# Performance work log

Hardware: AMD Instinct MI355X
Metric: run time of the kernel (lower is better)

## Reference

```python
import jax, jax.numpy as jnp
import numpy as np
import math

S = 72; IMG_W = 640; IMG_H = 360; STRIDE = 16
IN_CH = 256; AFC = 64
FMAP_H = IMG_H // STRIDE  # 22
FMAP_W = IMG_W // STRIDE  # 40
N_OFFSETS = S
LEFT_ANGLES = [72., 60., 49., 39., 30., 22.]
RIGHT_ANGLES = [108., 120., 131., 141., 150., 158.]
BOTTOM_ANGLES = [165., 150., 141., 131., 120., 108., 100., 90., 80., 72., 60., 49., 39., 30., 15.]
BATCH = 8


def _gen_anchor(start, angle, cut):
    n = FMAP_H if cut else N_OFFSETS
    ys = np.linspace(1., 0., n)
    a = np.zeros(5 + n)
    sx, sy = start
    a[2] = 1. - sy
    a[3] = sx
    a[5:] = (sx + (1. - ys - 1. + sy) / math.tan(angle * math.pi / 180.)) * IMG_W
    return a


def _gen_side(angles, nb, x=None, y=None):
    if x is None:
        starts = [(xx, y) for xx in np.linspace(1., 0., nb)]
    else:
        starts = [(x, yy) for yy in np.linspace(1., 0., nb)]
    anc = np.stack([_gen_anchor(s, a, False) for s in starts for a in angles])
    cut = np.stack([_gen_anchor(s, a, True) for s in starts for a in angles])
    return anc, cut


def build_anchor_tables():
    la, lc = _gen_side(LEFT_ANGLES, 72, x=0.)
    ra, rc = _gen_side(RIGHT_ANGLES, 72, x=1.)
    ba, bc = _gen_side(BOTTOM_ANGLES, 128, y=1.)
    anchors = np.concatenate([la, ba, ra]).astype(np.float32)  # [P, 5+S]
    cuts = np.concatenate([lc, bc, rc])                        # [P, 5+fmap_h]
    xs = np.flip(np.round(cuts[:, 5:] / STRIDE), axis=1).astype(np.int64)
    cut_xs = np.clip(xs, 0, FMAP_W - 1).astype(np.int32)       # [P, fmap_h]
    invalid = (xs < 0) | (xs > FMAP_W)                         # faithful to original (> not >=)
    return anchors, cut_xs, invalid


def setup_inputs():
    key = jax.random.key(0)
    ks = jax.random.split(key, 6)
    anchors, cut_xs, invalid = build_anchor_tables()
    P = anchors.shape[0]  # 2784
    D = AFC * FMAP_H      # 1408
    s = 0.02
    return {
        "x": jax.random.normal(ks[0], (BATCH, IN_CH, FMAP_H, FMAP_W), jnp.float32),
        "conv_w": jax.random.normal(ks[1], (AFC, IN_CH), jnp.float32) * s,
        "conv_b": jnp.zeros((AFC,), jnp.float32),
        "att_w": jax.random.normal(ks[2], (P - 1, D), jnp.float32) * s,
        "att_b": jnp.zeros((P - 1,), jnp.float32),
        "cls_w": jax.random.normal(ks[3], (2, 2 * D), jnp.float32) * s,
        "cls_b": jnp.zeros((2,), jnp.float32),
        "so_w": jax.random.normal(ks[4], (1, 2 * D), jnp.float32) * s,
        "so_b": jnp.zeros((1,), jnp.float32),
        "reg_w": jax.random.normal(ks[5], (N_OFFSETS + 1, 2 * D), jnp.float32) * s,
        "reg_b": jnp.zeros((N_OFFSETS + 1,), jnp.float32),
        "anchors": jnp.asarray(anchors),
        "cut_xs": jnp.asarray(cut_xs),
        "invalid_mask": jnp.asarray(invalid),
    }


def reference(x, conv_w, conv_b, att_w, att_b, cls_w, cls_b, so_w, so_b, reg_w, reg_b, anchors, cut_xs, invalid_mask):
    B = x.shape[0]
    P, H = cut_xs.shape
    # 1x1 conv
    feat = jnp.einsum('bchw,oc->bohw', x, conv_w) + conv_b[None, :, None, None]
    # fused anchor feature gather: rois[b,p,c,h] = feat[b,c,h,cut_xs[p,h]]
    rois = feat[:, :, jnp.arange(H)[None, :], cut_xs]           # [B,C,P,H]
    rois = jnp.transpose(rois, (0, 2, 1, 3))                    # [B,P,C,H]
    rois = jnp.where(invalid_mask[None, :, None, :], 0., rois)
    D = rois.shape[2] * H
    baf = rois.reshape(B, P, D)
    scores = baf.reshape(B * P, D) @ att_w.T + att_b
    attention = jax.nn.softmax(scores, axis=1).reshape(B, P, P - 1)
    # off-diagonal scatter (replaces torch eye/nonzero trick): M[b,i,j]=attention[b,i,j'] for j!=i, diag 0
    i_idx = jnp.arange(P)[:, None]
    j_off = jnp.arange(P - 1)[None, :]
    tgt_j = jnp.where(j_off < i_idx, j_off, j_off + 1)          # [P,P-1]
    M = jnp.zeros((B, P, P), x.dtype).at[:, jnp.broadcast_to(i_idx, (P, P - 1)), tgt_j].set(attention)
    # (baf^T @ M^T)^T == M @ baf
    att_feats = jnp.einsum('bpq,bqd->bpd', M, baf)
    feats = jnp.concatenate([att_feats, baf], axis=2).reshape(B * P, 2 * D)
    cls = (feats @ cls_w.T + cls_b).reshape(B, P, 2)
    so = jax.nn.sigmoid(feats @ so_w.T + so_b).reshape(B, P, 1)
    reg = (feats @ reg_w.T + reg_b).reshape(B, P, N_OFFSETS + 1)
    anc = jnp.broadcast_to(anchors[None], (B, P, anchors.shape[1]))
    reg_proposals = jnp.concatenate([cls, (anc[:, :, 2:3] + so) * 0.5, anc[:, :, 3:4], anc[:, :, 4:] + reg], axis=2)
    return reg_proposals, M, feat
```

## Files before the change

kernel.cpp:

```cpp
#include <hip/hip_runtime.h>
#include <stdint.h>

#define PTOT 2784
#define PM1  2783
#define DDIM 1408
#define NB   8
#define ROWS 22272
#define KHEAD 2816
#define MROW 2816
#define BTROWS 1536

typedef __attribute__((ext_vector_type(8))) short bf16x8;
typedef __attribute__((ext_vector_type(4))) float f32x4;
typedef long i64f8;

__device__ __forceinline__ short f2bf_rne(float x) {
    uint32_t u = __float_as_uint(x);
    u += 0x7fffu + ((u >> 16) & 1u);
    return (short)(u >> 16);
}
__device__ __forceinline__ float bf2f(short s) {
    return __uint_as_float((uint32_t)(unsigned short)s << 16);
}

__device__ __forceinline__ unsigned char f2e4m3(float x) {
    uint32_t u = __float_as_uint(x);
    uint32_t sgn = (u >> 24) & 0x80u;
    uint32_t ax = u & 0x7fffffffu;
    ax += 0x7ffffu + ((ax >> 20) & 1u);
    if (ax >= 0x43E80000u) return (unsigned char)(sgn | 0x7Eu);
    if (ax < 0x3C800000u) return (unsigned char)sgn;
    uint32_t e = (ax >> 23) - 120u;
    uint32_t m = (ax >> 20) & 7u;
    return (unsigned char)(sgn | (e << 3) | m);
}

__device__ __forceinline__ void gld16(const void* g, void* l) {
    __builtin_amdgcn_global_load_lds(
        (const __attribute__((address_space(1))) void*)(uintptr_t)g,
        (__attribute__((address_space(3))) void*)(uint32_t)(uintptr_t)l,
        16, 0, 0);
}

__global__ __launch_bounds__(256) void k_conv(
    const float* __restrict__ x, const float* __restrict__ w,
    const float* __restrict__ cb, float* __restrict__ feat) {
  __shared__ float xs[256 * 32];
  int b = blockIdx.x / 28;
  int t0 = (blockIdx.x % 28) * 32;
  int t = threadIdx.x;
  for (int i = t; i < 256 * 32; i += 256) {
    int c = i >> 5, pos = i & 31;
    int hw = t0 + pos;
    xs[i] = (hw < 880) ? x[((size_t)b * 256 + c) * 880 + hw] : 0.f;
  }
  __syncthreads();
  int o = t & 63, g = t >> 6;
  float acc[8];
#pragma unroll
  for (int pp = 0; pp < 8; ++pp) acc[pp] = cb[o];
  const float* wr = w + o * 256;
  for (int c = 0; c < 256; ++c) {
    float wv = wr[c];
#pragma unroll
    for (int pp = 0; pp < 8; ++pp) acc[pp] += wv * xs[c * 32 + g + pp * 4];
  }
#pragma unroll
  for (int pp = 0; pp < 8; ++pp) {
    int hw = t0 + g + pp * 4;
    if (hw < 880) feat[((size_t)b * 64 + o) * 880 + hw] = acc[pp];
  }
}

__global__ __launch_bounds__(256) void k_prep(
    const float* __restrict__ att_w, const float* __restrict__ cls_w,
    const float* __restrict__ so_w, const float* __restrict__ reg_w,
    const float* __restrict__ cls_b, const float* __restrict__ so_b,
    const float* __restrict__ reg_b,
    short* __restrict__ attw, short* __restrict__ wbf,
    float* __restrict__ bias80, float* __restrict__ M,
    unsigned char* __restrict__ Mbf8, unsigned char* __restrict__ bafT8,
    short* __restrict__ Msc) {
  const int64_t n_attw = (int64_t)2816 * DDIM;
  const int64_t n_w = 80 * (int64_t)KHEAD;
  const int64_t n_pa = (int64_t)NB * MROW * 32;
  const int64_t n_pb = (int64_t)NB * BTROWS * 32;
  const int64_t total = n_attw + n_w + 80 + ROWS + n_pa + n_pb;
  for (int64_t i = (int64_t)blockIdx.x * 256 + threadIdx.x; i < total;
       i += (int64_t)gridDim.x * 256) {
    if (i < n_attw) {
      int j = (int)(i / DDIM), k = (int)(i - (int64_t)j * DDIM);
      float v = (j < PM1) ? att_w[(size_t)j * DDIM + k] : 0.f;
      attw[i] = f2bf_rne(v);
    } else if (i < n_attw + n_w) {
      int64_t ii = i - n_attw;
      int n = (int)(ii / KHEAD), k = (int)(ii - (int64_t)n * KHEAD);
      float v = 0.f;
      if (n < 2) v = cls_w[n * KHEAD + k];
      else if (n == 2) v = so_w[k];
      else if (n < 76) v = reg_w[(size_t)(n - 3) * KHEAD + k];
      wbf[ii] = f2bf_rne(v);
    } else if (i < n_attw + n_w + 80) {
      int n = (int)(i - n_attw - n_w);
      float v = 0.f;
      if (n < 2) v = cls_b[n];
      else if (n == 2) v = so_b[0];
      else if (n < 76) v = reg_b[n - 3];
      bias80[n] = v;
    } else if (i < n_attw + n_w + 80 + ROWS) {
      int r = (int)(i - n_attw - n_w - 80);
      int p = r % PTOT;
      M[(size_t)r * PTOT + p] = -1e30f;
      if (Msc) Msc[(size_t)r * PTOT + p] = f2bf_rne(-1e30f);
    } else if (i < n_attw + n_w + 80 + ROWS + n_pa) {
      int64_t ii = i - n_attw - n_w - 80 - ROWS;
      int64_t row = ii >> 5; int c = (int)(ii & 31);
      Mbf8[row * 2816 + 2784 + c] = 0;
    } else {
      int64_t ii = i - n_attw - n_w - 80 - ROWS - n_pa;
      int64_t row = ii >> 5; int c = (int)(ii & 31);
      bafT8[row * 2816 + 2784 + c] = 0;
    }
  }
}

__global__ __launch_bounds__(256) void k_gather(
    const float* __restrict__ feat, const int* __restrict__ cutx,
    const unsigned char* __restrict__ inval,
    short* __restrict__ baf, unsigned char* __restrict__ bafT8) {
  int p0 = blockIdx.x * 64, d0 = blockIdx.y * 64, b = blockIdx.z;
  __shared__ short tile[64][72];
  int t = threadIdx.x;
  for (int i = t; i < 64 * 64; i += 256) {
    int pl = i >> 6, dl = i & 63;
    int p = p0 + pl, d = d0 + dl;
    float v = 0.f;
    if (p < PTOT && d < DDIM) {
      int c = d / 22, h = d - c * 22;
      if (!inval[p * 22 + h]) {
        int xc = cutx[p * 22 + h];
        v = feat[(((size_t)b * 64 + c) * 22 + h) * 40 + xc];
      }
    }
    tile[pl][dl] = f2bf_rne(v);
  }
  __syncthreads();
  if (d0 < DDIM) {
    for (int u = t; u < 512; u += 256) {
      int pl = u >> 3, dg = u & 7;
      int p = p0 + pl;
      if (p < PTOT) {
        bf16x8 v;
#pragma unroll
        for (int e = 0; e < 8; ++e) v[e] = tile[pl][dg * 8 + e];
        *(bf16x8*)&baf[((size_t)b * PTOT + p) * DDIM + d0 + dg * 8] = v;
      }
    }
  }
  for (int u = t; u < 512; u += 256) {
    int dl = u >> 3, pg = u & 7;
    int pbase = p0 + pg * 8;
    if (pbase + 7 < PTOT) {
      unsigned long long pk = 0;
#pragma unroll
      for (int e = 0; e < 8; ++e) {
        float fv = bf2f(tile[pg * 8 + e][dl]);
        pk |= (unsigned long long)f2e4m3(fv) << (8 * e);
      }
      *(unsigned long long*)&bafT8[((size_t)b * BTROWS + d0 + dl) * 2816 + pbase] = pk;
    }
  }
}

template<int OUTMODE>
__global__ __launch_bounds__(256) void k_scores(
    const short* __restrict__ baf, const short* __restrict__ attw,
    const float* __restrict__ att_b, float* __restrict__ Mout,
    short* __restrict__ Msc) {
  __shared__ char smA[8192];
  __shared__ char smB[8192];
  int wg = blockIdx.x;
  int xcd = wg & 7, lin = wg >> 3;
  int wgid = (xcd < 4) ? xcd * 479 + lin : 1916 + (xcd - 4) * 478 + lin;
  int it = wgid / 22, nt = wgid - it * 22;
  int m0 = it * 128, n0 = nt * 128;

  int t = threadIdx.x, w = t >> 6, l = t & 63;
  int lr = l & 15, lg = l >> 4;
  int wr = w >> 1, wc = w & 1;

  const char* gA[2]; const char* gB[2]; int dd[2];
#pragma unroll
  for (int c = 0; c < 2; ++c) {
    int o = w * 2048 + c * 1024 + l * 16;
    int row = o >> 6;
    int colb = (o & 63) ^ (((o >> 7) & 3) << 4);
    gA[c] = (const char*)(baf + (size_t)(m0 + row) * DDIM) + colb;
    gB[c] = (const char*)(attw + (size_t)(n0 + row) * DDIM) + colb;
    dd[c] = o;
  }
  int offA[4], offB[4];
#pragma unroll
  for (int i = 0; i < 4; ++i) {
    int xa = (wr * 64 + i * 16 + lr) * 64 + lg * 16;
    offA[i] = xa ^ (((xa >> 7) & 3) << 4);
    int xb = (wc * 64 + i * 16 + lr) * 64 + lg * 16;
    offB[i] = xb ^ (((xb >> 7) & 3) << 4);
  }

  f32x4 acc[4][4];
  const f32x4 fz = {0.f, 0.f, 0.f, 0.f};
#pragma unroll
  for (int mi = 0; mi < 4; ++mi)
#pragma unroll
    for (int ni = 0; ni < 4; ++ni) acc[mi][ni] = fz;

  for (int kt = 0; kt < 44; ++kt) {
    gld16(gA[0] + (size_t)kt * 64, smA + dd[0]);
    gld16(gA[1] + (size_t)kt * 64, smA + dd[1]);
    gld16(gB[0] + (size_t)kt * 64, smB + dd[0]);
    gld16(gB[1] + (size_t)kt * 64, smB + dd[1]);
    __syncthreads();
    bf16x8 av[4], bv[4];
#pragma unroll
    for (int i = 0; i < 4; ++i) av[i] = *(const bf16x8*)(smA + offA[i]);
#pragma unroll
    for (int i = 0; i < 4; ++i) bv[i] = *(const bf16x8*)(smB + offB[i]);
#pragma unroll
    for (int mi = 0; mi < 4; ++mi)
#pragma unroll
      for (int ni = 0; ni < 4; ++ni)
        acc[mi][ni] = __builtin_amdgcn_mfma_f32_16x16x32_bf16(
            av[mi], bv[ni], acc[mi][ni], 0, 0, 0);
    __syncthreads();
  }

#pragma unroll
  for (int mi = 0; mi < 4; ++mi) {
#pragma unroll
    for (int rg = 0; rg < 4; ++rg) {
      int gmi = m0 + wr * 64 + mi * 16 + lg * 4 + rg;
      int i = gmi % PTOT;
#pragma unroll
      for (int ni = 0; ni < 4; ++ni) {
        int j = n0 + wc * 64 + ni * 16 + lr;
        if (j < PM1) {
          int q2 = j + (j >= i);
          float v = acc[mi][ni][rg] + att_b[j];
          if (OUTMODE == 0) Mout[(size_t)gmi * PTOT + q2] = v;
          else              Msc[(size_t)gmi * PTOT + q2] = f2bf_rne(v);
        }
      }
    }
  }
}

__global__ __launch_bounds__(256) void k_attfeat8(
    const unsigned char* __restrict__ Mbf8,
    const unsigned char* __restrict__ bafT8,
    short* __restrict__ attf) {
  __shared__ char smA[8192];
  __shared__ char smB[8192];
  int wg = blockIdx.x;
  int wgid = (wg & 7) * 242 + (wg >> 3);
  int bb = wgid / 242;
  int rem = wgid - bb * 242;
  int it = rem / 11, nt = rem - it * 11;
  int m0 = it * 128, n0 = nt * 128;
  const unsigned char* Ab = Mbf8 + ((size_t)bb * MROW + m0) * 2816;
  const unsigned char* Bb = bafT8 + ((size_t)bb * BTROWS + n0) * 2816;

  int t = threadIdx.x, w = t >> 6, l = t & 63;
  int lr = l & 15, lg = l >> 4;
  int wr = w >> 1, wc = w & 1;

  const char* gA[2]; const char* gB[2]; int dd[2];
#pragma unroll
  for (int c = 0; c < 2; ++c) {
    int o = c * 4096 + t * 16;
    int row = o >> 6;
    int colb = (o & 63) ^ (((o >> 7) & 3) << 4);
    gA[c] = (const char*)Ab + (size_t)row * 2816 + colb;
    gB[c] = (const char*)Bb + (size_t)row * 2816 + colb;
    dd[c] = o;
  }
  int offA[8], offB[8];
#pragma unroll
  for (int i = 0; i < 4; ++i) {
#pragma unroll
    for (int ks = 0; ks < 2; ++ks) {
      int xa = (wr * 64 + i * 16 + lr) * 64 + ks * 32 + lg * 8;
      offA[i * 2 + ks] = xa ^ (((xa >> 7) & 3) << 4);
      int xb = (wc * 64 + i * 16 + lr) * 64 + ks * 32 + lg * 8;
      offB[i * 2 + ks] = xb ^ (((xb >> 7) & 3) << 4);
    }
  }

  f32x4 acc[4][4];
  const f32x4 fz = {0.f, 0.f, 0.f, 0.f};
#pragma unroll
  for (int mi = 0; mi < 4; ++mi)
#pragma unroll
    for (int ni = 0; ni < 4; ++ni) acc[mi][ni] = fz;

  for (int kt = 0; kt < 44; ++kt) {
    gld16(gA[0] + (size_t)kt * 64, smA + dd[0]);
    gld16(gA[1] + (size_t)kt * 64, smA + dd[1]);
    gld16(gB[0] + (size_t)kt * 64, smB + dd[0]);
    gld16(gB[1] + (size_t)kt * 64, smB + dd[1]);
    __syncthreads();
#pragma unroll
    for (int ks = 0; ks < 2; ++ks) {
      i64f8 av[4], bv[4];
#pragma unroll
      for (int i = 0; i < 4; ++i) av[i] = *(const i64f8*)(smA + offA[i * 2 + ks]);
#pragma unroll
      for (int i = 0; i < 4; ++i) bv[i] = *(const i64f8*)(smB + offB[i * 2 + ks]);
#pragma unroll
      for (int mi = 0; mi < 4; ++mi)
#pragma unroll
        for (int ni = 0; ni < 4; ++ni)
          acc[mi][ni] = __builtin_amdgcn_mfma_f32_16x16x32_fp8_fp8(
              av[mi], bv[ni], acc[mi][ni], 0, 0, 0);
    }
    __syncthreads();
  }

  const float US = 1.0f / 1024.0f;
#pragma unroll
  for (int mi = 0; mi < 4; ++mi) {
#pragma unroll
    for (int rg = 0; rg < 4; ++rg) {
      int i = m0 + wr * 64 + mi * 16 + lg * 4 + rg;
      if (i < PTOT) {
        short* arow = attf + ((size_t)(bb * PTOT + i)) * DDIM + n0 + wc * 64;
#pragma unroll
        for (int ni = 0; ni < 4; ++ni)
          arow[ni * 16 + lr] = f2bf_rne(acc[mi][ni][rg] * US);
      }
    }
  }
}

template<int INMODE>
__global__ __launch_bounds__(256) void k_softmax(float* __restrict__ M,
                                                 unsigned char* __restrict__ Mbf8,
                                                 const short* __restrict__ Msc) {
  __shared__ float red[8];
  int r = blockIdx.x;
  int b = r / PTOT, p = r - b * PTOT;
  float* pr = M + (size_t)r * PTOT;
  const short* ms = INMODE ? (Msc + (size_t)r * PTOT) : (const short*)nullptr;
  unsigned char* mb = Mbf8 + ((size_t)b * MROW + p) * 2816;
  int t = threadIdx.x;
  bool has2 = (t < 348 - 256);
  float v0[8], v1[8];
  float mx = -3.0e38f;
  if (INMODE == 0) {
    f32x4 a0 = *(const f32x4*)(pr + t * 8);
    f32x4 a1 = *(const f32x4*)(pr + t * 8 + 4);
#pragma unroll
    for (int e = 0; e < 4; ++e) { v0[e] = a0[e]; v0[4 + e] = a1[e]; }
  } else {
    bf16x8 a = *(const bf16x8*)(ms + t * 8);
#pragma unroll
    for (int e = 0; e < 8; ++e) v0[e] = bf2f(a[e]);
  }
#pragma unroll
  for (int e = 0; e < 8; ++e) mx = fmaxf(mx, v0[e]);
  if (has2) {
    if (INMODE == 0) {
      f32x4 b0 = *(const f32x4*)(pr + (256 + t) * 8);
      f32x4 b1 = *(const f32x4*)(pr + (256 + t) * 8 + 4);
#pragma unroll
      for (int e = 0; e < 4; ++e) { v1[e] = b0[e]; v1[4 + e] = b1[e]; }
    } else {
      bf16x8 bb = *(const bf16x8*)(ms + (256 + t) * 8);
#pragma unroll
      for (int e = 0; e < 8; ++e) v1[e] = bf2f(bb[e]);
    }
#pragma unroll
    for (int e = 0; e < 8; ++e) mx = fmaxf(mx, v1[e]);
  }
#pragma unroll
  for (int off = 32; off; off >>= 1) mx = fmaxf(mx, __shfl_xor(mx, off));
  if ((t & 63) == 0) red[t >> 6] = mx;
  __syncthreads();
  mx = fmaxf(fmaxf(red[0], red[1]), fmaxf(red[2], red[3]));
  float s = 0.f;
#pragma unroll
  for (int e = 0; e < 8; ++e) { v0[e] = __expf(v0[e] - mx); s += v0[e]; }
  if (has2) {
#pragma unroll
    for (int e = 0; e < 8; ++e) { v1[e] = __expf(v1[e] - mx); s += v1[e]; }
  }
#pragma unroll
  for (int off = 32; off; off >>= 1) s += __shfl_xor(s, off);
  if ((t & 63) == 0) red[4 + (t >> 6)] = s;
  __syncthreads();
  s = (red[4] + red[5]) + (red[6] + red[7]);
  float inv = 1.f / s;
  float invs = inv * 1024.f;
  {
    f32x4 o0, o1; unsigned long long pk = 0;
#pragma unroll
    for (int e = 0; e < 8; ++e) {
      float wv = v0[e] * inv;
      if (e < 4) o0[e] = wv; else o1[e - 4] = wv;
      pk |= (unsigned long long)f2e4m3(v0[e] * invs) << (8 * e);
    }
    *(f32x4*)(pr + t * 8) = o0;
    *(f32x4*)(pr + t * 8 + 4) = o1;
    *(unsigned long long*)(mb + t * 8) = pk;
  }
  if (has2) {
    f32x4 o0, o1; unsigned long long pk = 0;
#pragma unroll
    for (int e = 0; e < 8; ++e) {
      float wv = v1[e] * inv;
      if (e < 4) o0[e] = wv; else o1[e - 4] = wv;
      pk |= (unsigned long long)f2e4m3(v1[e] * invs) << (8 * e);
    }
    *(f32x4*)(pr + (256 + t) * 8) = o0;
    *(f32x4*)(pr + (256 + t) * 8 + 4) = o1;
    *(unsigned long long*)(mb + (256 + t) * 8) = pk;
  }
}

__global__ __launch_bounds__(256) void k_head(
    const short* __restrict__ attf, const short* __restrict__ baf,
    const short* __restrict__ wbf, const float* __restrict__ bias80,
    const float* __restrict__ anch, float* __restrict__ out) {
  __shared__ short smA[64 * 32];
  __shared__ short smB[80 * 32];
  int r0 = blockIdx.x * 64;
  int t = threadIdx.x, wid = t >> 6, lane = t & 63;
  int rowa = t >> 2, kg = t & 3;
  const short* sA_att = attf + (size_t)(r0 + rowa) * DDIM + kg * 8;
  const short* sA_baf = baf + (size_t)(r0 + rowa) * DDIM + kg * 8;
  const short* sB0 = wbf + (size_t)rowa * KHEAD + kg * 8;
  const short* sB1 = wbf + (size_t)(64 + (t >> 2)) * KHEAD + (t & 3) * 8;
  char* lA = (char*)smA + wid * 1024;
  char* lB0 = (char*)smB + wid * 1024;
  char* lB1 = (char*)smB + 4096;
  int lr = lane & 15, lg = lane >> 4;
  const short* pA = smA + (wid * 16 + lr) * 32 + lg * 8;
  const short* pB = smB + lr * 32 + lg * 8;
  f32x4 acc[5];
  const f32x4 fz = {0.f, 0.f, 0.f, 0.f};
  for (int i2 = 0; i2 < 5; ++i2) acc[i2] = fz;
  for (int ks = 0; ks < 88; ++ks) {
    const short* sA = (ks < 44) ? (sA_att + ks * 32) : (sA_baf + (ks - 44) * 32);
    gld16(sA, lA);
    gld16(sB0 + ks * 32, lB0);
    if (t < 64) gld16(sB1 + ks * 32, lB1);
    __syncthreads();
    bf16x8 a = *(const bf16x8*)pA;
#pragma unroll
    for (int ni = 0; ni < 5; ++ni) {
      bf16x8 b = *(const bf16x8*)(pB + ni * 512);
      acc[ni] = __builtin_amdgcn_mfma_f32_16x16x32_bf16(a, b, acc[ni], 0, 0, 0);
    }
    __syncthreads();
  }
#pragma unroll
  for (int ni = 0; ni < 5; ++ni) {
#pragma unroll
    for (int rg = 0; rg < 4; ++rg) {
      int n = ni * 16 + lr;
      int i = wid * 16 + lg * 4 + rg;
      int rgl = r0 + i;
      int p = rgl % PTOT;
      float v = acc[ni][rg] + bias80[n];
      if (n < 2) {
        out[(size_t)rgl * 77 + n] = v;
      } else if (n == 2) {
        out[(size_t)rgl * 77 + 2] =
            (anch[(size_t)p * 77 + 2] + 1.f / (1.f + __expf(-v))) * 0.5f;
        out[(size_t)rgl * 77 + 3] = anch[(size_t)p * 77 + 3];
      } else if (n < 76) {
        out[(size_t)rgl * 77 + n + 1] = v + anch[(size_t)p * 77 + n + 1];
      }
    }
  }
}

extern "C" void kernel_launch(void* const* d_in, const int* in_sizes, int n_in,
                              void* d_out, int out_size, void* d_ws, size_t ws_size,
                              hipStream_t stream) {
  const float* x      = (const float*)d_in[0];
  const float* conv_w = (const float*)d_in[1];
  const float* conv_b = (const float*)d_in[2];
  const float* att_w  = (const float*)d_in[3];
  const float* att_b  = (const float*)d_in[4];
  const float* cls_w  = (const float*)d_in[5];
  const float* cls_b  = (const float*)d_in[6];
  const float* so_w   = (const float*)d_in[7];
  const float* so_b   = (const float*)d_in[8];
  const float* reg_w  = (const float*)d_in[9];
  const float* reg_b  = (const float*)d_in[10];
  const float* anchors= (const float*)d_in[11];
  const int*   cut_xs = (const int*)d_in[12];
  const unsigned char* invalid = (const unsigned char*)d_in[13];

  float* out_rp = (float*)d_out;
  float* Mmat = out_rp + (size_t)ROWS * 77;
  float* feat = Mmat + (size_t)ROWS * PTOT;

  char* wsp = (char*)d_ws;
  short* baf            = (short*)wsp;
  unsigned char* bafT8  = (unsigned char*)(wsp + 62717952ULL);
  unsigned char* Mbf8   = (unsigned char*)(wsp + 97320960ULL);
  short* attw           = (short*)(wsp + 160759808ULL);
  short* wbf            = (short*)(wsp + 168689664ULL);
  float* bias80         = (float*)(wsp + 169140224ULL);
  short* attf           = (short*)(wsp + 169140736ULL);
  short* Msc            = (short*)(wsp + 231858688ULL);
  const size_t WS_FAST  = 231858688ULL + 124010496ULL;

  bool fast = (ws_size >= WS_FAST);

  k_conv<<<224, 256, 0, stream>>>(x, conv_w, conv_b, feat);
  k_prep<<<2048, 256, 0, stream>>>(att_w, cls_w, so_w, reg_w, cls_b, so_b, reg_b,
                                   attw, wbf, bias80, Mmat, Mbf8, bafT8,
                                   fast ? Msc : (short*)nullptr);
  k_gather<<<dim3(44, 24, 8), 256, 0, stream>>>(feat, cut_xs, invalid, baf, bafT8);
  if (fast) {
    k_scores<1><<<3828, 256, 0, stream>>>(baf, attw, att_b, (float*)nullptr, Msc);
    k_softmax<1><<<ROWS, 256, 0, stream>>>(Mmat, Mbf8, Msc);
  } else {
    k_scores<0><<<3828, 256, 0, stream>>>(baf, attw, att_b, Mmat, (short*)nullptr);
    k_softmax<0><<<ROWS, 256, 0, stream>>>(Mmat, Mbf8, (const short*)nullptr);
  }
  k_attfeat8<<<1936, 256, 0, stream>>>(Mbf8, bafT8, attf);
  k_head<<<348, 256, 0, stream>>>(attf, baf, wbf, bias80, anchors, out_rp);
}
```

Measured before the change: 705.1 us.

## Triple-buffer LDS with prefetch depth two in scores and attfeat GEMMs

Replaces the single-buffered load-then-compute loops of the bf16 scores GEMM and the fp8 attention-feature GEMM with a three-stage LDS ring. Each iteration issues loads for the tile two steps ahead, then waits on vmcnt for the current tile before an explicit barrier and the MFMAs. This is meant to hide global-to-LDS latency behind compute instead of stalling on every tile. The cost is LDS growing from 16KB to 48KB per block, which may lower occupancy, and it depends on hand-counted vmcnt values being right.

Result: faster. 682.9 us (-3.1%).

```diff
diff --git a/kernel.cpp b/kernel.cpp
--- a/kernel.cpp
+++ b/kernel.cpp
@@ -41,6 +41,8 @@
         (__attribute__((address_space(3))) void*)(uint32_t)(uintptr_t)l,
         16, 0, 0);
 }
+
+#define VMW(N) asm volatile("s_waitcnt vmcnt(" #N ")" ::: "memory")
 
 __global__ __launch_bounds__(256) void k_conv(
     const float* __restrict__ x, const float* __restrict__ w,
@@ -172,13 +174,37 @@
   }
 }
 
+#define SC_TILE(T_, STAGE_, VM_)                                               \
+  {                                                                            \
+    const char* cb_ = sm + scur * 16384;                                       \
+    if (STAGE_) {                                                              \
+      char* nb_ = sm + snxt * 16384;                                           \
+      gld16(gA[0] + (size_t)((T_) + 2) * 64, nb_ + dd[0]);                     \
+      gld16(gA[1] + (size_t)((T_) + 2) * 64, nb_ + dd[1]);                     \
+      gld16(gB[0] + (size_t)((T_) + 2) * 64, nb_ + 8192 + dd[0]);              \
+      gld16(gB[1] + (size_t)((T_) + 2) * 64, nb_ + 8192 + dd[1]);              \
+    }                                                                          \
+    if ((VM_) == 8) VMW(8); else if ((VM_) == 4) VMW(4); else VMW(0);          \
+    __builtin_amdgcn_s_barrier();                                              \
+    bf16x8 av[4], bv[4];                                                       \
+    _Pragma("unroll") for (int i = 0; i < 4; ++i)                              \
+      av[i] = *(const bf16x8*)(cb_ + offA[i]);                                 \
+    _Pragma("unroll") for (int i = 0; i < 4; ++i)                              \
+      bv[i] = *(const bf16x8*)(cb_ + 8192 + offB[i]);                          \
+    _Pragma("unroll") for (int mi = 0; mi < 4; ++mi)                           \
+      _Pragma("unroll") for (int ni = 0; ni < 4; ++ni)                         \
+        acc[mi][ni] = __builtin_amdgcn_mfma_f32_16x16x32_bf16(                 \
+            av[mi], bv[ni], acc[mi][ni], 0, 0, 0);                             \
+    __builtin_amdgcn_s_barrier();                                              \
+    scur = snxt0_; snxt0_ = snxt; snxt = (snxt == 2) ? 0 : snxt + 1;           \
+  }
+
 template<int OUTMODE>
 __global__ __launch_bounds__(256) void k_scores(
     const short* __restrict__ baf, const short* __restrict__ attw,
     const float* __restrict__ att_b, float* __restrict__ Mout,
     short* __restrict__ Msc) {
-  __shared__ char smA[8192];
-  __shared__ char smB[8192];
+  __shared__ char sm[49152];
   int wg = blockIdx.x;
   int xcd = wg & 7, lin = wg >> 3;
   int wgid = (xcd < 4) ? xcd * 479 + lin : 1916 + (xcd - 4) * 478 + lin;
@@ -215,25 +241,18 @@
 #pragma unroll
     for (int ni = 0; ni < 4; ++ni) acc[mi][ni] = fz;
 
-  for (int kt = 0; kt < 44; ++kt) {
-    gld16(gA[0] + (size_t)kt * 64, smA + dd[0]);
-    gld16(gA[1] + (size_t)kt * 64, smA + dd[1]);
-    gld16(gB[0] + (size_t)kt * 64, smB + dd[0]);
-    gld16(gB[1] + (size_t)kt * 64, smB + dd[1]);
-    __syncthreads();
-    bf16x8 av[4], bv[4];
-#pragma unroll
-    for (int i = 0; i < 4; ++i) av[i] = *(const bf16x8*)(smA + offA[i]);
-#pragma unroll
-    for (int i = 0; i < 4; ++i) bv[i] = *(const bf16x8*)(smB + offB[i]);
-#pragma unroll
-    for (int mi = 0; mi < 4; ++mi)
-#pragma unroll
-      for (int ni = 0; ni < 4; ++ni)
-        acc[mi][ni] = __builtin_amdgcn_mfma_f32_16x16x32_bf16(
-            av[mi], bv[ni], acc[mi][ni], 0, 0, 0);
-    __syncthreads();
-  }
+#pragma unroll
+  for (int pt = 0; pt < 2; ++pt) {
+    gld16(gA[0] + (size_t)pt * 64, sm + pt * 16384 + dd[0]);
+    gld16(gA[1] + (size_t)pt * 64, sm + pt * 16384 + dd[1]);
+    gld16(gB[0] + (size_t)pt * 64, sm + pt * 16384 + 8192 + dd[0]);
+    gld16(gB[1] + (size_t)pt * 64, sm + pt * 16384 + 8192 + dd[1]);
+  }
+  int scur = 0, snxt0_ = 1, snxt = 2;
+  int kt = 0;
+  for (; kt < 42; ++kt) { SC_TILE(kt, 1, 8); }
+  SC_TILE(kt, 0, 4); ++kt;
+  SC_TILE(kt, 0, 0);
 
 #pragma unroll
   for (int mi = 0; mi < 4; ++mi) {
@@ -255,12 +274,38 @@
   }
 }
 
+#define AF_TILE(T_, STAGE_, VM_)                                               \
+  {                                                                            \
+    const char* cb_ = sm + scur * 16384;                                       \
+    if (STAGE_) {                                                              \
+      char* nb_ = sm + snxt * 16384;                                           \
+      gld16(gA[0] + (size_t)((T_) + 2) * 64, nb_ + dd[0]);                     \
+      gld16(gA[1] + (size_t)((T_) + 2) * 64, nb_ + dd[1]);                     \
+      gld16(gB[0] + (size_t)((T_) + 2) * 64, nb_ + 8192 + dd[0]);              \
+      gld16(gB[1] + (size_t)((T_) + 2) * 64, nb_ + 8192 + dd[1]);              \
+    }                                                                          \
+    if ((VM_) == 8) VMW(8); else if ((VM_) == 4) VMW(4); else VMW(0);          \
+    __builtin_amdgcn_s_barrier();                                              \
+    _Pragma("unroll") for (int ks = 0; ks < 2; ++ks) {                         \
+      i64f8 av[4], bv[4];                                                      \
+      _Pragma("unroll") for (int i = 0; i < 4; ++i)                            \
+        av[i] = *(const i64f8*)(cb_ + offA[i * 2 + ks]);                       \
+      _Pragma("unroll") for (int i = 0; i < 4; ++i)                            \
+        bv[i] = *(const i64f8*)(cb_ + 8192 + offB[i * 2 + ks]);                \
+      _Pragma("unroll") for (int mi = 0; mi < 4; ++mi)                         \
+        _Pragma("unroll") for (int ni = 0; ni < 4; ++ni)                       \
+          acc[mi][ni] = __builtin_amdgcn_mfma_f32_16x16x32_fp8_fp8(            \
+              av[mi], bv[ni], acc[mi][ni], 0, 0, 0);                           \
+    }                                                                          \
+    __builtin_amdgcn_s_barrier();                                              \
+    scur = snxt0_; snxt0_ = snxt; snxt = (snxt == 2) ? 0 : snxt + 1;           \
+  }
+
 __global__ __launch_bounds__(256) void k_attfeat8(
     const unsigned char* __restrict__ Mbf8,
     const unsigned char* __restrict__ bafT8,
     short* __restrict__ attf) {
-  __shared__ char smA[8192];
-  __shared__ char smB[8192];
+  __shared__ char sm[49152];
   int wg = blockIdx.x;
   int wgid = (wg & 7) * 242 + (wg >> 3);
   int bb = wgid / 242;
@@ -303,28 +348,18 @@
 #pragma unroll
     for (int ni = 0; ni < 4; ++ni) acc[mi][ni] = fz;
 
-  for (int kt = 0; kt < 44; ++kt) {
-    gld16(gA[0] + (size_t)kt * 64, smA + dd[0]);
-    gld16(gA[1] + (size_t)kt * 64, smA + dd[1]);
-    gld16(gB[0] + (size_t)kt * 64, smB + dd[0]);
-    gld16(gB[1] + (size_t)kt * 64, smB + dd[1]);
-    __syncthreads();
-#pragma unroll
-    for (int ks = 0; ks < 2; ++ks) {
-      i64f8 av[4], bv[4];
-#pragma unroll
-      for (int i = 0; i < 4; ++i) av[i] = *(const i64f8*)(smA + offA[i * 2 + ks]);
-#pragma unroll
-      for (int i = 0; i < 4; ++i) bv[i] = *(const i64f8*)(smB + offB[i * 2 + ks]);
-#pragma unroll
-      for (int mi = 0; mi < 4; ++mi)
-#pragma unroll
-        for (int ni = 0; ni < 4; ++ni)
-          acc[mi][ni] = __builtin_amdgcn_mfma_f32_16x16x32_fp8_fp8(
-              av[mi], bv[ni], acc[mi][ni], 0, 0, 0);
-    }
-    __syncthreads();
-  }
+#pragma unroll
+  for (int pt = 0; pt < 2; ++pt) {
+    gld16(gA[0] + (size_t)pt * 64, sm + pt * 16384 + dd[0]);
+    gld16(gA[1] + (size_t)pt * 64, sm + pt * 16384 + dd[1]);
+    gld16(gB[0] + (size_t)pt * 64, sm + pt * 16384 + 8192 + dd[0]);
+    gld16(gB[1] + (size_t)pt * 64, sm + pt * 16384 + 8192 + dd[1]);
+  }
+  int scur = 0, snxt0_ = 1, snxt = 2;
+  int kt = 0;
+  for (; kt < 42; ++kt) { AF_TILE(kt, 1, 8); }
+  AF_TILE(kt, 0, 4); ++kt;
+  AF_TILE(kt, 0, 0);
 
   const float US = 1.0f / 1024.0f;
 #pragma unroll
```
